# Kernel tuning notes

Hardware: AMD Instinct MI355X
Metric: run time of the kernel (lower is better)

Reference implementation:

```python
import jax, jax.numpy as jnp
import numpy as np

B, S, D = 8, 2048, 512
E, DF = 16, 2048  # total experts, FFN hidden (4*d_model)
K = 4             # num_available_experts


def setup_inputs() -> dict:
    key = jax.random.key(0)
    ks = jax.random.split(key, 5)
    scale = 0.02
    return {
        "x": jax.random.normal(ks[0], (B, S, D), dtype=jnp.float32),
        "gate_w": jax.random.normal(ks[1], (E, D), dtype=jnp.float32) * scale,
        "gate_b": jnp.zeros((E,), dtype=jnp.float32),
        "w1": jax.random.normal(ks[2], (E, D, DF), dtype=jnp.float32) * scale,
        "b1": jnp.zeros((E, DF), dtype=jnp.float32),
        "w2": jax.random.normal(ks[3], (E, DF, D), dtype=jnp.float32) * scale,
        "b2": jnp.zeros((E, D), dtype=jnp.float32),
        "num_available": K,
    }


def reference(x, gate_w, gate_b, w1, b1, w2, b2, num_available):
    # Coarse expert selection: gate applied to the global token sum k = sum_{b,s} x
    k = jnp.sum(x, axis=(0, 1))                       # [D]
    coarse = gate_w @ k + gate_b                      # [E]
    _, idx = jax.lax.top_k(coarse, num_available)     # [K]

    # Gather selected experts' params
    gw_w, gw_b = gate_w[idx], gate_b[idx]             # [K,D], [K]
    W1, B1 = w1[idx], b1[idx]                         # [K,D,DF], [K,DF]
    W2, B2 = w2[idx], b2[idx]                         # [K,DF,D], [K,D]

    # Per-token softmax gating over the K selected experts
    logits = jnp.einsum('bsd,kd->bsk', x, gw_w) + gw_b  # [B,S,K]
    gw = jax.nn.softmax(logits, axis=2)                 # [B,S,K]

    # Dense expert FFNs over all tokens, weighted combine
    h = jax.nn.gelu(jnp.einsum('bsd,kdf->kbsf', x, W1) + B1[:, None, None, :])  # [K,B,S,DF]
    eo = jnp.einsum('kbsf,kfd->kbsd', h, W2) + B2[:, None, None, :]             # [K,B,S,D]
    out = jnp.einsum('kbsd,bsk->bsd', eo, gw)                                   # [B,S,D]
    return out
```

## Files before the change

### kernel.cpp

```cpp
#include <hip/hip_runtime.h>
#include <hip/hip_bf16.h>
#include <cstdint>
#include <cstddef>

typedef __attribute__((ext_vector_type(8))) short short8;
typedef __attribute__((ext_vector_type(4))) float f32x4;

#define AS1U32(p) ((const __attribute__((address_space(1))) uint32_t*)(p))
#define AS3U32(p) ((__attribute__((address_space(3))) uint32_t*)(p))

__device__ __forceinline__ unsigned short f2bf(float v) {
  union { float f; uint32_t u; } a; a.f = v;
  uint32_t u = a.u;
  u += 0x7FFFu + ((u >> 16) & 1u);
  return (unsigned short)(u >> 16);
}

__device__ __forceinline__ float gelu_fast(float x) {
  const float c0 = 0.7978845608028654f;
  const float c1 = 0.044715f;
  float u = c0 * (x + c1 * x * x * x);
  return x * __builtin_amdgcn_rcpf(1.0f + __expf(-2.0f * u));
}


__global__ __launch_bounds__(512)
void reduce_part(const float* __restrict__ x, float* __restrict__ kpart) {
  const int d = threadIdx.x;
  const int b = blockIdx.x;
  float s = 0.f;
#pragma unroll 4
  for (int i = 0; i < 64; i++)
    s += x[((size_t)b * 64 + i) * 512 + d];
  kpart[(size_t)b * 512 + d] = s;
}

__global__ __launch_bounds__(1024)
void gate_all(const float* __restrict__ kpart,
              const float* __restrict__ gate_w,
              const float* __restrict__ gate_b,
              const float* __restrict__ b1, const float* __restrict__ b2,
              int* __restrict__ idxout,
              float* __restrict__ b1cat, float* __restrict__ b2sel) {
  __shared__ float ksum2[2][512];
  __shared__ float coarse[16];
  __shared__ int idxl[4];
  const int t = threadIdx.x;
  {
    const int d = t & 511, h = t >> 9;
    float s = 0.f;
    for (int p = h * 128; p < h * 128 + 128; p++) s += kpart[(size_t)p * 512 + d];
    ksum2[h][d] = s;
  }
  __syncthreads();
  {
    const int wave = t >> 6, lane = t & 63;
    const int d0 = lane * 8;
    float s = 0.f;
#pragma unroll
    for (int j = 0; j < 8; j++)
      s += gate_w[wave * 512 + d0 + j] * (ksum2[0][d0 + j] + ksum2[1][d0 + j]);
#pragma unroll
    for (int off = 32; off >= 1; off >>= 1) s += __shfl_down(s, off, 64);
    if (lane == 0) coarse[wave] = s + gate_b[wave];
  }
  __syncthreads();
  if (t == 0) {
    unsigned taken = 0;
    for (int r = 0; r < 4; r++) {
      float best = -3.4e38f; int bi = 0;
      for (int e = 0; e < 16; e++)
        if (!((taken >> e) & 1u) && coarse[e] > best) { best = coarse[e]; bi = e; }
      taken |= 1u << bi;
      idxl[r] = bi; idxout[r] = bi;
    }
  }
  __syncthreads();
  for (int i = t; i < 8192; i += 1024)
    b1cat[i] = b1[(size_t)idxl[i >> 11] * 2048 + (i & 2047)];
  for (int i = t; i < 2048; i += 1024)
    b2sel[i] = b2[(size_t)idxl[i >> 9] * 512 + (i & 511)];
}

__global__ __launch_bounds__(256)
void transpose_all(const float* __restrict__ w1, const float* __restrict__ w2,
                   unsigned short* __restrict__ w1t, unsigned short* __restrict__ w2t,
                   const int* __restrict__ idx) {
  __shared__ float tl[64][65];
  const int tid = threadIdx.x;
  const int ty = tid >> 6, tx = tid & 63;
  const int z = blockIdx.z;
  const float* src; unsigned short* dbase; int C, dstLd, r0, c0;
  if (z < 4) {
    src = w1 + (size_t)idx[z] * 512 * 2048;
    dbase = w1t + (size_t)z * 2048 * 512;
    C = 2048; dstLd = 512;
    r0 = blockIdx.x * 64; c0 = blockIdx.y * 64;
  } else {
    src = w2 + (size_t)idx[z - 4] * 2048 * 512;
    dbase = w2t + (size_t)(z - 4) * 2048;
    C = 512; dstLd = 8192;
    r0 = blockIdx.y * 64; c0 = blockIdx.x * 64;
  }
#pragma unroll
  for (int i = 0; i < 16; i++) {
    int r = ty * 16 + i;
    tl[r][tx] = src[(size_t)(r0 + r) * C + c0 + tx];
  }
  __syncthreads();
#pragma unroll
  for (int i = 0; i < 16; i++) {
    int rr = ty * 16 + i;
    dbase[(size_t)(c0 + rr) * dstLd + r0 + tx] = f2bf(tl[tx][rr]);
  }
}

__global__ __launch_bounds__(256)
void gate_softmax_xconv(const float* __restrict__ x,
                        const float* __restrict__ gate_w,
                        const float* __restrict__ gate_b,
                        const int* __restrict__ idx,
                        float* __restrict__ gwout,
                        unsigned short* __restrict__ xbf) {
  __shared__ float wsel[4][512];
  __shared__ float bsel[4];
  const int tid = threadIdx.x;
  for (int i = tid; i < 2048; i += 256) {
    int k = i >> 9;
    wsel[k][i & 511] = gate_w[(size_t)idx[k] * 512 + (i & 511)];
  }
  if (tid < 4) bsel[tid] = gate_b[idx[tid]];
  __syncthreads();
  const int wave = tid >> 6, lane = tid & 63;
  const int t = blockIdx.x * 4 + wave;
  const float* xr = x + (size_t)t * 512 + lane * 8;
  float4 v0 = ((const float4*)xr)[0];
  float4 v1 = ((const float4*)xr)[1];
  float vals[8] = {v0.x, v0.y, v0.z, v0.w, v1.x, v1.y, v1.z, v1.w};
  short8 pk;
#pragma unroll
  for (int j = 0; j < 8; j++) pk[j] = (short)f2bf(vals[j]);
  *(short8*)(xbf + (size_t)t * 512 + lane * 8) = pk;
  float a0 = 0.f, a1 = 0.f, a2 = 0.f, a3 = 0.f;
  const int dbase = lane * 8;
#pragma unroll
  for (int j = 0; j < 8; j++) {
    float xv = vals[j];
    a0 += xv * wsel[0][dbase + j];
    a1 += xv * wsel[1][dbase + j];
    a2 += xv * wsel[2][dbase + j];
    a3 += xv * wsel[3][dbase + j];
  }
#pragma unroll
  for (int off = 32; off >= 1; off >>= 1) {
    a0 += __shfl_down(a0, off, 64);
    a1 += __shfl_down(a1, off, 64);
    a2 += __shfl_down(a2, off, 64);
    a3 += __shfl_down(a3, off, 64);
  }
  if (lane == 0) {
    float l0 = a0 + bsel[0], l1 = a1 + bsel[1], l2 = a2 + bsel[2], l3 = a3 + bsel[3];
    float m = fmaxf(fmaxf(l0, l1), fmaxf(l2, l3));
    float e0 = __expf(l0 - m), e1 = __expf(l1 - m);
    float e2 = __expf(l2 - m), e3 = __expf(l3 - m);
    float inv = 1.0f / (e0 + e1 + e2 + e3);
    float* o = gwout + (size_t)t * 4;
    o[0] = e0 * inv; o[1] = e1 * inv; o[2] = e2 * inv; o[3] = e3 * inv;
  }
}

template <int EPI>
__global__ __launch_bounds__(256, 2)
void gemm_bt(const unsigned short* __restrict__ A,
             const unsigned short* __restrict__ Bt,
             void* __restrict__ C, int K, int lda, int ldb, int ldc,
             const float* __restrict__ gw,
             const float* __restrict__ bias, int colOff, int accum) {
  __shared__ unsigned short lA[128 * 64];
  __shared__ unsigned short lB[128 * 64];
  const int tid = threadIdx.x;
  const int wave = tid >> 6;
  const int lane = tid & 63;
  const int rowA0 = blockIdx.x * 128;
  const int rowB0 = blockIdx.y * 128;

  f32x4 acc[4][4];
#pragma unroll
  for (int i = 0; i < 4; i++)
#pragma unroll
    for (int j = 0; j < 4; j++) acc[i][j] = (f32x4){0.f, 0.f, 0.f, 0.f};

  const int lrow = lane >> 3;
  const int lslot = lane & 7;
  const int gchunk = lslot ^ lrow;
  const int fr = lane & 15;
  const int quad = lane >> 4;
  const int wm = (wave >> 1) * 64;
  const int wn = (wave & 1) * 64;
  const int swz = fr & 7;

  for (int kt = 0; kt < K; kt += 64) {
#pragma unroll
    for (int c = 0; c < 4; c++) {
      int r = wave * 32 + c * 8 + lrow;
      const unsigned short* gp = A + (size_t)(rowA0 + r) * lda + kt + gchunk * 8;
      __builtin_amdgcn_global_load_lds(AS1U32(gp), AS3U32(lA + (wave * 32 + c * 8) * 64), 16, 0, 0);
    }
#pragma unroll
    for (int c = 0; c < 4; c++) {
      int r = wave * 32 + c * 8 + lrow;
      const unsigned short* gp = Bt + (size_t)(rowB0 + r) * ldb + kt + gchunk * 8;
      __builtin_amdgcn_global_load_lds(AS1U32(gp), AS3U32(lB + (wave * 32 + c * 8) * 64), 16, 0, 0);
    }
    __syncthreads();
#pragma unroll
    for (int ks = 0; ks < 2; ks++) {
      short8 af[4], bfr[4];
      const int c = ks * 4 + quad;
      const int slot = (c ^ swz) << 3;
#pragma unroll
      for (int i = 0; i < 4; i++)
        af[i] = *(const short8*)(lA + (wm + i * 16 + fr) * 64 + slot);
#pragma unroll
      for (int j = 0; j < 4; j++)
        bfr[j] = *(const short8*)(lB + (wn + j * 16 + fr) * 64 + slot);
#pragma unroll
      for (int i = 0; i < 4; i++)
#pragma unroll
        for (int j = 0; j < 4; j++)
          acc[i][j] = __builtin_amdgcn_mfma_f32_16x16x32_bf16(af[i], bfr[j], acc[i][j], 0, 0, 0);
    }
    __syncthreads();
  }

  if (EPI == 1) {
    unsigned short* Cb = (unsigned short*)C;
    const int kexp = (colOff + rowB0) >> 11;
#pragma unroll
    for (int i = 0; i < 4; i++) {
#pragma unroll
      for (int reg = 0; reg < 4; reg++) {
        int r = rowA0 + wm + i * 16 + quad * 4 + reg;
        float g = gw[(size_t)r * 4 + kexp];
#pragma unroll
        for (int j = 0; j < 4; j++) {
          int n = rowB0 + wn + j * 16 + fr;
          float v = acc[i][j][reg] + bias[colOff + n];
          Cb[(size_t)r * ldc + n] = f2bf(gelu_fast(v) * g);
        }
      }
    }
  } else {
    float* Cf = (float*)C;
#pragma unroll
    for (int i = 0; i < 4; i++) {
#pragma unroll
      for (int reg = 0; reg < 4; reg++) {
        int r = rowA0 + wm + i * 16 + quad * 4 + reg;
        size_t t4 = (size_t)r * 4;
        float g0 = gw[t4], g1 = gw[t4 + 1], g2 = gw[t4 + 2], g3 = gw[t4 + 3];
#pragma unroll
        for (int j = 0; j < 4; j++) {
          int n = rowB0 + wn + j * 16 + fr;
          size_t ci = (size_t)r * 512 + n;
          float v = acc[i][j][reg];
          if (accum) v += Cf[ci];
          else v += g0 * bias[n] + g1 * bias[512 + n] +
                    g2 * bias[1024 + n] + g3 * bias[1536 + n];
          Cf[ci] = v;
        }
      }
    }
  }
}


extern "C" void kernel_launch(void* const* d_in, const int* in_sizes, int n_in,
                              void* d_out, int out_size, void* d_ws, size_t ws_size,
                              hipStream_t stream) {
  (void)in_sizes; (void)n_in; (void)out_size;
  const float* x      = (const float*)d_in[0];
  const float* gate_w = (const float*)d_in[1];
  const float* gate_b = (const float*)d_in[2];
  const float* w1     = (const float*)d_in[3];
  const float* b1     = (const float*)d_in[4];
  const float* w2     = (const float*)d_in[5];
  const float* b2     = (const float*)d_in[6];

  char* ws = (char*)d_ws;
  int*            idx   = (int*)(ws + 0);
  float*          gw    = (float*)(ws + 4096);
  float*          b1cat = (float*)(ws + 266240);
  float*          b2sel = (float*)(ws + 299008);
  float*          kpart = (float*)(ws + 307200);
  unsigned short* xbf   = (unsigned short*)(ws + 831488);
  unsigned short* w1t   = (unsigned short*)(ws + 17608704);
  unsigned short* w2t   = (unsigned short*)(ws + 25997312);
  unsigned short* hbuf  = (unsigned short*)(ws + 34385920);
  const size_t HBUF_OFF = 34385920;

  size_t avail = ws_size > HBUF_OFF ? ws_size - HBUF_OFF : 0;
  int nslab = 1;
  while (nslab < 16 && (size_t)16384 * (8192 / nslab) * 2 > avail) nslab <<= 1;
  const int slabDF = 8192 / nslab;

  reduce_part<<<256, 512, 0, stream>>>(x, kpart);
  gate_all<<<1, 1024, 0, stream>>>(kpart, gate_w, gate_b, b1, b2, idx, b1cat, b2sel);
  transpose_all<<<dim3(8, 32, 8), 256, 0, stream>>>(w1, w2, w1t, w2t, idx);
  gate_softmax_xconv<<<4096, 256, 0, stream>>>(x, gate_w, gate_b, idx, gw, xbf);

  for (int s = 0; s < nslab; s++) {
    const int c0 = s * slabDF;
    gemm_bt<1><<<dim3(128, slabDF / 128), 256, 0, stream>>>(
        xbf, w1t + (size_t)c0 * 512, hbuf,
        512, 512, 512, slabDF,
        gw, b1cat, c0, 0);
    gemm_bt<2><<<dim3(128, 4), 256, 0, stream>>>(
        hbuf, w2t + c0, (float*)d_out,
        slabDF, slabDF, 8192, 512,
        gw, b2sel, 0, s > 0);
  }
}
```

Measured before the change: 525.0 us.

## Merge prep kernels and give second GEMM a smaller 64x128 tile

The weight-transpose kernel and the gate-softmax/x-conversion kernel become one launch that branches on block index, saving a launch and letting the two stages overlap. The second GEMM gets its own kernel with a 64-row tile and a 256x4 grid instead of 128x4. That doubles the workgroup count to fill more CUs for an output only 512 wide. Smaller tiles reload the B operand more often, and the merged kernel's shared-memory use is the larger of the two branches, which may limit occupancy.

```diff
diff --git a/kernel.cpp b/kernel.cpp
--- a/kernel.cpp
+++ b/kernel.cpp
@@ -83,99 +83,97 @@
 }
 
 __global__ __launch_bounds__(256)
-void transpose_all(const float* __restrict__ w1, const float* __restrict__ w2,
-                   unsigned short* __restrict__ w1t, unsigned short* __restrict__ w2t,
-                   const int* __restrict__ idx) {
-  __shared__ float tl[64][65];
+void prep_all(const float* __restrict__ w1, const float* __restrict__ w2,
+              unsigned short* __restrict__ w1t, unsigned short* __restrict__ w2t,
+              const float* __restrict__ x,
+              const float* __restrict__ gate_w,
+              const float* __restrict__ gate_b,
+              const int* __restrict__ idx,
+              float* __restrict__ gwout,
+              unsigned short* __restrict__ xbf) {
   const int tid = threadIdx.x;
-  const int ty = tid >> 6, tx = tid & 63;
-  const int z = blockIdx.z;
-  const float* src; unsigned short* dbase; int C, dstLd, r0, c0;
-  if (z < 4) {
-    src = w1 + (size_t)idx[z] * 512 * 2048;
-    dbase = w1t + (size_t)z * 2048 * 512;
-    C = 2048; dstLd = 512;
-    r0 = blockIdx.x * 64; c0 = blockIdx.y * 64;
+  const int bid = blockIdx.x;
+  if (bid < 2048) {
+    __shared__ float tl[64][65];
+    const int ty = tid >> 6, tx = tid & 63;
+    const int z = bid >> 8, bx = (bid >> 5) & 7, by = bid & 31;
+    const float* src; unsigned short* dbase; int C, dstLd, r0, c0;
+    if (z < 4) {
+      src = w1 + (size_t)idx[z] * 512 * 2048;
+      dbase = w1t + (size_t)z * 2048 * 512;
+      C = 2048; dstLd = 512;
+      r0 = bx * 64; c0 = by * 64;
+    } else {
+      src = w2 + (size_t)idx[z - 4] * 2048 * 512;
+      dbase = w2t + (size_t)(z - 4) * 2048;
+      C = 512; dstLd = 8192;
+      r0 = by * 64; c0 = bx * 64;
+    }
+#pragma unroll
+    for (int i = 0; i < 16; i++) {
+      int r = ty * 16 + i;
+      tl[r][tx] = src[(size_t)(r0 + r) * C + c0 + tx];
+    }
+    __syncthreads();
+#pragma unroll
+    for (int i = 0; i < 16; i++) {
+      int rr = ty * 16 + i;
+      dbase[(size_t)(c0 + rr) * dstLd + r0 + tx] = f2bf(tl[tx][rr]);
+    }
   } else {
-    src = w2 + (size_t)idx[z - 4] * 2048 * 512;
-    dbase = w2t + (size_t)(z - 4) * 2048;
-    C = 512; dstLd = 8192;
-    r0 = blockIdx.y * 64; c0 = blockIdx.x * 64;
-  }
-#pragma unroll
-  for (int i = 0; i < 16; i++) {
-    int r = ty * 16 + i;
-    tl[r][tx] = src[(size_t)(r0 + r) * C + c0 + tx];
-  }
-  __syncthreads();
-#pragma unroll
-  for (int i = 0; i < 16; i++) {
-    int rr = ty * 16 + i;
-    dbase[(size_t)(c0 + rr) * dstLd + r0 + tx] = f2bf(tl[tx][rr]);
-  }
-}
-
-__global__ __launch_bounds__(256)
-void gate_softmax_xconv(const float* __restrict__ x,
-                        const float* __restrict__ gate_w,
-                        const float* __restrict__ gate_b,
-                        const int* __restrict__ idx,
-                        float* __restrict__ gwout,
-                        unsigned short* __restrict__ xbf) {
-  __shared__ float wsel[4][512];
-  __shared__ float bsel[4];
-  const int tid = threadIdx.x;
-  for (int i = tid; i < 2048; i += 256) {
-    int k = i >> 9;
-    wsel[k][i & 511] = gate_w[(size_t)idx[k] * 512 + (i & 511)];
-  }
-  if (tid < 4) bsel[tid] = gate_b[idx[tid]];
-  __syncthreads();
-  const int wave = tid >> 6, lane = tid & 63;
-  const int t = blockIdx.x * 4 + wave;
-  const float* xr = x + (size_t)t * 512 + lane * 8;
-  float4 v0 = ((const float4*)xr)[0];
-  float4 v1 = ((const float4*)xr)[1];
-  float vals[8] = {v0.x, v0.y, v0.z, v0.w, v1.x, v1.y, v1.z, v1.w};
-  short8 pk;
-#pragma unroll
-  for (int j = 0; j < 8; j++) pk[j] = (short)f2bf(vals[j]);
-  *(short8*)(xbf + (size_t)t * 512 + lane * 8) = pk;
-  float a0 = 0.f, a1 = 0.f, a2 = 0.f, a3 = 0.f;
-  const int dbase = lane * 8;
-#pragma unroll
-  for (int j = 0; j < 8; j++) {
-    float xv = vals[j];
-    a0 += xv * wsel[0][dbase + j];
-    a1 += xv * wsel[1][dbase + j];
-    a2 += xv * wsel[2][dbase + j];
-    a3 += xv * wsel[3][dbase + j];
-  }
-#pragma unroll
-  for (int off = 32; off >= 1; off >>= 1) {
-    a0 += __shfl_down(a0, off, 64);
-    a1 += __shfl_down(a1, off, 64);
-    a2 += __shfl_down(a2, off, 64);
-    a3 += __shfl_down(a3, off, 64);
-  }
-  if (lane == 0) {
-    float l0 = a0 + bsel[0], l1 = a1 + bsel[1], l2 = a2 + bsel[2], l3 = a3 + bsel[3];
-    float m = fmaxf(fmaxf(l0, l1), fmaxf(l2, l3));
-    float e0 = __expf(l0 - m), e1 = __expf(l1 - m);
-    float e2 = __expf(l2 - m), e3 = __expf(l3 - m);
-    float inv = 1.0f / (e0 + e1 + e2 + e3);
-    float* o = gwout + (size_t)t * 4;
-    o[0] = e0 * inv; o[1] = e1 * inv; o[2] = e2 * inv; o[3] = e3 * inv;
-  }
-}
-
-template <int EPI>
+    __shared__ float wsel[4][512];
+    __shared__ float bsel[4];
+    for (int i = tid; i < 2048; i += 256) {
+      int k = i >> 9;
+      wsel[k][i & 511] = gate_w[(size_t)idx[k] * 512 + (i & 511)];
+    }
+    if (tid < 4) bsel[tid] = gate_b[idx[tid]];
+    __syncthreads();
+    const int wave = tid >> 6, lane = tid & 63;
+    const int t = (bid - 2048) * 4 + wave;
+    const float* xr = x + (size_t)t * 512 + lane * 8;
+    float4 v0 = ((const float4*)xr)[0];
+    float4 v1 = ((const float4*)xr)[1];
+    float vals[8] = {v0.x, v0.y, v0.z, v0.w, v1.x, v1.y, v1.z, v1.w};
+    short8 pk;
+#pragma unroll
+    for (int j = 0; j < 8; j++) pk[j] = (short)f2bf(vals[j]);
+    *(short8*)(xbf + (size_t)t * 512 + lane * 8) = pk;
+    float a0 = 0.f, a1 = 0.f, a2 = 0.f, a3 = 0.f;
+    const int dbase = lane * 8;
+#pragma unroll
+    for (int j = 0; j < 8; j++) {
+      float xv = vals[j];
+      a0 += xv * wsel[0][dbase + j];
+      a1 += xv * wsel[1][dbase + j];
+      a2 += xv * wsel[2][dbase + j];
+      a3 += xv * wsel[3][dbase + j];
+    }
+#pragma unroll
+    for (int off = 32; off >= 1; off >>= 1) {
+      a0 += __shfl_down(a0, off, 64);
+      a1 += __shfl_down(a1, off, 64);
+      a2 += __shfl_down(a2, off, 64);
+      a3 += __shfl_down(a3, off, 64);
+    }
+    if (lane == 0) {
+      float l0 = a0 + bsel[0], l1 = a1 + bsel[1], l2 = a2 + bsel[2], l3 = a3 + bsel[3];
+      float m = fmaxf(fmaxf(l0, l1), fmaxf(l2, l3));
+      float e0 = __expf(l0 - m), e1 = __expf(l1 - m);
+      float e2 = __expf(l2 - m), e3 = __expf(l3 - m);
+      float inv = 1.0f / (e0 + e1 + e2 + e3);
+      float* o = gwout + (size_t)t * 4;
+      o[0] = e0 * inv; o[1] = e1 * inv; o[2] = e2 * inv; o[3] = e3 * inv;
+    }
+  }
+}
+
 __global__ __launch_bounds__(256, 2)
-void gemm_bt(const unsigned short* __restrict__ A,
-             const unsigned short* __restrict__ Bt,
-             void* __restrict__ C, int K, int lda, int ldb, int ldc,
-             const float* __restrict__ gw,
-             const float* __restrict__ bias, int colOff, int accum) {
+void gemm1(const unsigned short* __restrict__ A,
+           const unsigned short* __restrict__ Bt,
+           unsigned short* __restrict__ Cb, int K, int lda, int ldb, int ldc,
+           const float* __restrict__ gw,
+           const float* __restrict__ bias, int colOff) {
   __shared__ unsigned short lA[128 * 64];
   __shared__ unsigned short lB[128 * 64];
   const int tid = threadIdx.x;
@@ -233,42 +231,102 @@
     __syncthreads();
   }
 
-  if (EPI == 1) {
-    unsigned short* Cb = (unsigned short*)C;
-    const int kexp = (colOff + rowB0) >> 11;
-#pragma unroll
-    for (int i = 0; i < 4; i++) {
-#pragma unroll
-      for (int reg = 0; reg < 4; reg++) {
-        int r = rowA0 + wm + i * 16 + quad * 4 + reg;
-        float g = gw[(size_t)r * 4 + kexp];
-#pragma unroll
-        for (int j = 0; j < 4; j++) {
-          int n = rowB0 + wn + j * 16 + fr;
-          float v = acc[i][j][reg] + bias[colOff + n];
-          Cb[(size_t)r * ldc + n] = f2bf(gelu_fast(v) * g);
-        }
+  const int kexp = (colOff + rowB0) >> 11;
+#pragma unroll
+  for (int i = 0; i < 4; i++) {
+#pragma unroll
+    for (int reg = 0; reg < 4; reg++) {
+      int r = rowA0 + wm + i * 16 + quad * 4 + reg;
+      float g = gw[(size_t)r * 4 + kexp];
+#pragma unroll
+      for (int j = 0; j < 4; j++) {
+        int n = rowB0 + wn + j * 16 + fr;
+        float v = acc[i][j][reg] + bias[colOff + n];
+        Cb[(size_t)r * ldc + n] = f2bf(gelu_fast(v) * g);
       }
     }
-  } else {
-    float* Cf = (float*)C;
-#pragma unroll
-    for (int i = 0; i < 4; i++) {
-#pragma unroll
-      for (int reg = 0; reg < 4; reg++) {
-        int r = rowA0 + wm + i * 16 + quad * 4 + reg;
-        size_t t4 = (size_t)r * 4;
-        float g0 = gw[t4], g1 = gw[t4 + 1], g2 = gw[t4 + 2], g3 = gw[t4 + 3];
-#pragma unroll
-        for (int j = 0; j < 4; j++) {
-          int n = rowB0 + wn + j * 16 + fr;
-          size_t ci = (size_t)r * 512 + n;
-          float v = acc[i][j][reg];
-          if (accum) v += Cf[ci];
-          else v += g0 * bias[n] + g1 * bias[512 + n] +
-                    g2 * bias[1024 + n] + g3 * bias[1536 + n];
-          Cf[ci] = v;
-        }
+  }
+}
+
+__global__ __launch_bounds__(256)
+void gemm2(const unsigned short* __restrict__ A,
+           const unsigned short* __restrict__ Bt,
+           float* __restrict__ Cf, int K, int lda, int ldb,
+           const float* __restrict__ gw,
+           const float* __restrict__ bias, int accum) {
+  __shared__ unsigned short lA[64 * 64];
+  __shared__ unsigned short lB[128 * 64];
+  const int tid = threadIdx.x;
+  const int wave = tid >> 6;
+  const int lane = tid & 63;
+  const int rowA0 = blockIdx.x * 64;
+  const int rowB0 = blockIdx.y * 128;
+
+  f32x4 acc[2][4];
+#pragma unroll
+  for (int i = 0; i < 2; i++)
+#pragma unroll
+    for (int j = 0; j < 4; j++) acc[i][j] = (f32x4){0.f, 0.f, 0.f, 0.f};
+
+  const int lrow = lane >> 3;
+  const int lslot = lane & 7;
+  const int gchunk = lslot ^ lrow;
+  const int fr = lane & 15;
+  const int quad = lane >> 4;
+  const int wm = (wave >> 1) * 32;
+  const int wn = (wave & 1) * 64;
+  const int swz = fr & 7;
+
+  for (int kt = 0; kt < K; kt += 64) {
+#pragma unroll
+    for (int c = 0; c < 2; c++) {
+      int r = wave * 16 + c * 8 + lrow;
+      const unsigned short* gp = A + (size_t)(rowA0 + r) * lda + kt + gchunk * 8;
+      __builtin_amdgcn_global_load_lds(AS1U32(gp), AS3U32(lA + (wave * 16 + c * 8) * 64), 16, 0, 0);
+    }
+#pragma unroll
+    for (int c = 0; c < 4; c++) {
+      int r = wave * 32 + c * 8 + lrow;
+      const unsigned short* gp = Bt + (size_t)(rowB0 + r) * ldb + kt + gchunk * 8;
+      __builtin_amdgcn_global_load_lds(AS1U32(gp), AS3U32(lB + (wave * 32 + c * 8) * 64), 16, 0, 0);
+    }
+    __syncthreads();
+#pragma unroll
+    for (int ks = 0; ks < 2; ks++) {
+      short8 af[2], bfr[4];
+      const int c = ks * 4 + quad;
+      const int slot = (c ^ swz) << 3;
+#pragma unroll
+      for (int i = 0; i < 2; i++)
+        af[i] = *(const short8*)(lA + (wm + i * 16 + fr) * 64 + slot);
+#pragma unroll
+      for (int j = 0; j < 4; j++)
+        bfr[j] = *(const short8*)(lB + (wn + j * 16 + fr) * 64 + slot);
+#pragma unroll
+      for (int i = 0; i < 2; i++)
+#pragma unroll
+        for (int j = 0; j < 4; j++)
+          acc[i][j] = __builtin_amdgcn_mfma_f32_16x16x32_bf16(af[i], bfr[j], acc[i][j], 0, 0, 0);
+    }
+    __syncthreads();
+  }
+
+#pragma unroll
+  for (int i = 0; i < 2; i++) {
+#pragma unroll
+    for (int reg = 0; reg < 4; reg++) {
+      int r = rowA0 + wm + i * 16 + quad * 4 + reg;
+      size_t t4 = (size_t)r * 4;
+      float g0 = gw[t4], g1 = gw[t4 + 1], g2 = gw[t4 + 2], g3 = gw[t4 + 3];
+#pragma unroll
+      for (int j = 0; j < 4; j++) {
+        int n = rowB0 + wn + j * 16 + fr;
+        size_t ci = (size_t)r * 512 + n;
+        float v = acc[i][j][reg];
+        if (accum) v += Cf[ci];
+        else v += g0 * bias[n] + g1 * bias[512 + n] +
+                  g2 * bias[1024 + n] + g3 * bias[1536 + n];
+        Cf[ci] = v;
       }
     }
   }
@@ -306,18 +364,17 @@
 
   reduce_part<<<256, 512, 0, stream>>>(x, kpart);
   gate_all<<<1, 1024, 0, stream>>>(kpart, gate_w, gate_b, b1, b2, idx, b1cat, b2sel);
-  transpose_all<<<dim3(8, 32, 8), 256, 0, stream>>>(w1, w2, w1t, w2t, idx);
-  gate_softmax_xconv<<<4096, 256, 0, stream>>>(x, gate_w, gate_b, idx, gw, xbf);
+  prep_all<<<6144, 256, 0, stream>>>(w1, w2, w1t, w2t, x, gate_w, gate_b, idx, gw, xbf);
 
   for (int s = 0; s < nslab; s++) {
     const int c0 = s * slabDF;
-    gemm_bt<1><<<dim3(128, slabDF / 128), 256, 0, stream>>>(
+    gemm1<<<dim3(128, slabDF / 128), 256, 0, stream>>>(
         xbf, w1t + (size_t)c0 * 512, hbuf,
         512, 512, 512, slabDF,
-        gw, b1cat, c0, 0);
-    gemm_bt<2><<<dim3(128, 4), 256, 0, stream>>>(
+        gw, b1cat, c0);
+    gemm2<<<dim3(256, 4), 256, 0, stream>>>(
         hbuf, w2t + c0, (float*)d_out,
-        slabDF, slabDF, 8192, 512,
-        gw, b2sel, 0, s > 0);
-  }
-}
+        slabDF, slabDF, 8192,
+        gw, b2sel, s > 0);
+  }
+}
```

Result: no change. 527.1 us (+0.4%).
